# Optimization experiments

Hardware: AMD Instinct MI355X
Metric: run time of the kernel (lower is better)

Reference implementation:

```python
import jax, jax.numpy as jnp
import numpy as np

KERNEL_MUL = 2.0
KERNEL_NUM = 5


def setup_inputs() -> dict:
    key = jax.random.key(0)
    k1, k2 = jax.random.split(key)
    B, Ns, Nt, K = 4, 2048, 2048, 32
    source = jax.random.normal(k1, (B, Ns, K), dtype=jnp.float32)
    target = jax.random.normal(k2, (B, Nt, K), dtype=jnp.float32)
    return {"source": source, "target": target}


def _mmd_rbf(source, target):
    # source: [B, Ns, K], target: [B, Nt, K]
    Ns = source.shape[1]
    Nt = target.shape[1]
    n_samples = Ns + Nt
    total = jnp.concatenate([source, target], axis=1)  # [B, N, K]
    # Pairwise squared L2 via Gram trick (avoids [B, N, N, K] broadcast tensor)
    sq = jnp.sum(total * total, axis=-1)  # [B, N]
    gram = jnp.einsum('bik,bjk->bij', total, total)  # [B, N, N]
    L2 = sq[:, :, None] + sq[:, None, :] - 2.0 * gram  # [B, N, N]
    # Multi-bandwidth RBF kernel sum
    bw = jnp.sum(L2, axis=(1, 2), keepdims=True) / (n_samples ** 2 - n_samples + 1e-8)  # [B,1,1]
    bw = bw / (KERNEL_MUL ** (KERNEL_NUM // 2))
    # Small fixed loop over bandwidths; accumulate to avoid [K_num, B, N, N] stack.
    kernel = jnp.zeros_like(L2)
    for i in range(KERNEL_NUM):
        kernel = kernel + jnp.exp(-L2 / (bw * (KERNEL_MUL ** i)) + 1e-8)
    # Quadrant means
    N = Ns
    XX = kernel[:, :N, :N].mean(axis=(1, 2))
    YY = kernel[:, N:, N:].mean(axis=(1, 2))
    XY = kernel[:, :N, N:].mean(axis=(1, 2))
    YX = kernel[:, N:, :N].mean(axis=(1, 2))
    return XX + YY - XY - YX  # [B]


def reference(source, target):
    return _mmd_rbf(source, target)
```

## Files before the change

kernel.cpp:

```cpp
#include <hip/hip_runtime.h>
#include <hip/hip_bf16.h>


#define NPTS 4096
#define HALF 2048
#define KDIM 32
#define T3   128
#define NTB3 32
#define GRIDX 187
#define SPREAD 64

#define WS_SQ    0
#define WS_PART  65536
#define WS_QUAD  133120
#define WS_FRAG  147456
#define WS_NEED  (147456 + 4 * NPTS * 128)

typedef __attribute__((ext_vector_type(8))) short short8v;
typedef __attribute__((ext_vector_type(4))) float f32x4;

__device__ __forceinline__ float fast_exp2(float x) {
#if __has_builtin(__builtin_amdgcn_exp2f)
  return __builtin_amdgcn_exp2f(x);
#else
  return exp2f(x);
#endif
}

__device__ __forceinline__ unsigned int bf16_rne(float x) {
  unsigned int u = __float_as_uint(x);
  return (u + 0x7fffu + ((u >> 16) & 1u)) >> 16;
}

__device__ __forceinline__ const float* point_ptr(const float* __restrict__ src,
                                                  const float* __restrict__ tgt,
                                                  int b, int p) {
  return (p < HALF) ? src + ((size_t)b * HALF + p) * KDIM
                    : tgt + ((size_t)b * HALF + (p - HALF)) * KDIM;
}

__global__ void __launch_bounds__(64)
mmd_pass1(const float* __restrict__ src, const float* __restrict__ tgt,
          float* __restrict__ sqArr, double* __restrict__ part1,
          double* __restrict__ quadbuf,
          unsigned char* __restrict__ frags, int preFlag) {
  const int b = blockIdx.y;
  const int tid = threadIdx.x;
  const int p = blockIdx.x * 64 + tid;

  if (blockIdx.x == 0) {
#pragma unroll
    for (int i = 0; i < 4; ++i)
      quadbuf[b * 4 * SPREAD + i * 64 + tid] = 0.0;
  }

  const float* __restrict__ xp = point_ptr(src, tgt, b, p);
  float x[KDIM];
#pragma unroll
  for (int q = 0; q < 8; ++q) {
    float4 v = reinterpret_cast<const float4*>(xp)[q];
    x[4*q+0] = v.x; x[4*q+1] = v.y; x[4*q+2] = v.z; x[4*q+3] = v.w;
  }
  float s0 = 0.f, s1 = 0.f, s2 = 0.f, s3 = 0.f;
#pragma unroll
  for (int q = 0; q < 8; ++q) {
    s0 = fmaf(x[4*q+0], x[4*q+0], s0);
    s1 = fmaf(x[4*q+1], x[4*q+1], s1);
    s2 = fmaf(x[4*q+2], x[4*q+2], s2);
    s3 = fmaf(x[4*q+3], x[4*q+3], s3);
  }
  const float sq = (s0 + s1) + (s2 + s3);
  sqArr[(size_t)b * NPTS + p] = sq;

  if (preFlag) {
    unsigned int hw[16], lw[16];
#pragma unroll
    for (int e = 0; e < 16; ++e) {
      const float xa = x[2*e], xb = x[2*e+1];
      const unsigned int ha = bf16_rne(xa);
      const unsigned int la = bf16_rne(xa - __uint_as_float(ha << 16));
      const unsigned int hb = bf16_rne(xb);
      const unsigned int lb = bf16_rne(xb - __uint_as_float(hb << 16));
      hw[e] = ha | (hb << 16);
      lw[e] = la | (lb << 16);
    }
    uint4* dst = reinterpret_cast<uint4*>(frags + (size_t)(b * NPTS + p) * 128);
#pragma unroll
    for (int c = 0; c < 4; ++c)
      dst[c] = make_uint4(hw[4*c], hw[4*c+1], hw[4*c+2], hw[4*c+3]);
#pragma unroll
    for (int c = 0; c < 4; ++c)
      dst[4 + c] = make_uint4(lw[4*c], lw[4*c+1], lw[4*c+2], lw[4*c+3]);
  }

  __shared__ float lx[64][KDIM + 1];
#pragma unroll
  for (int k = 0; k < KDIM; ++k) lx[tid][k] = x[k];
  __syncthreads();

  double* slot = part1 + ((size_t)b * 64 + blockIdx.x) * 33;
  if (tid < 32) {
    float ps = 0.f;
#pragma unroll 16
    for (int r = 0; r < 64; ++r) ps += lx[r][tid];
    slot[1 + tid] = (double)ps;
  }
  float w = sq;
#pragma unroll
  for (int off = 32; off > 0; off >>= 1) w += __shfl_down(w, off, 64);
  if (tid == 0) slot[0] = (double)w;
}

__device__ __forceinline__ short8v lds_frag(const unsigned char* base, int p,
                                            int half, int lk) {
  const int slot = (half * 4 + lk) ^ (p & 7);
  return *reinterpret_cast<const short8v*>(base + p * 128 + slot * 16);
}

template <bool PRE>
__global__ void __launch_bounds__(512, 6)
mmd_pass3(const float* __restrict__ src, const float* __restrict__ tgt,
          const float* __restrict__ sqArr, const double* __restrict__ part1,
          const unsigned char* __restrict__ frags,
          double* __restrict__ quadbuf) {
  const int bid = blockIdx.x;
  const int b = blockIdx.y;
  const int tid = threadIdx.x;
  const int lane = tid & 63;
  const int w = tid >> 6;
  const int lm = lane & 15;
  const int lk = lane >> 4;
  const int wr = w & 3;
  const int wc = w >> 2;

  int rem = bid, bx = 0;
  for (;;) {
    const int nseg = (32 - bx + 2) / 3;
    if (rem < nseg) break;
    rem -= nseg; ++bx;
  }
  const int by0 = bx + rem * 3;
  const int cnt = min(3, 32 - by0);

  __shared__ __align__(16) unsigned char fragA[T3 * 128];
  __shared__ __align__(16) unsigned char fragB[2][T3 * 128];
  __shared__ float s_sqA[T3], s_sqB[2][T3];
  __shared__ double red[33];
  __shared__ float s_nc4;

  const float* __restrict__ sqG = sqArr + (size_t)b * NPTS;
  const uint4* __restrict__ gfr =
      reinterpret_cast<const uint4*>(frags) + (size_t)b * NPTS * 8;

  if (tid < 33) {
    double s = 0.0;
#pragma unroll 16
    for (int blk = 0; blk < 64; ++blk)
      s += part1[((size_t)b * 64 + blk) * 33 + tid];
    red[tid] = s;
  }
  __syncthreads();
  if (tid == 0) {
    double ssq = red[0], s2 = 0.0;
    for (int k = 1; k <= 32; ++k) s2 += red[k] * red[k];
    const double N = (double)NPTS;
    double bw = (2.0 * N * ssq - 2.0 * s2) / (N * N - N + 1e-8);
    bw *= 0.25;
    s_nc4 = (float)(-1.4426950408889634 / (bw * 16.0));
  }

  if constexpr (PRE) {
#pragma unroll
    for (int i = 0; i < 2; ++i) {
      const int g = tid + i * 512;
      const int p = g >> 3, s = g & 7;
      const int d = p * 8 + (s ^ (p & 7));
      reinterpret_cast<uint4*>(fragA)[d] = gfr[(size_t)bx * 1024 + g];
      reinterpret_cast<uint4*>(fragB[0])[d] = gfr[(size_t)by0 * 1024 + g];
    }
  } else if (tid < 256) {
    const int pt = tid & 127;
    const bool isB = tid >= 128;
    const float* fp = point_ptr(src, tgt, b, (isB ? by0 : bx) * T3 + pt);
    unsigned int hw[16], lw[16];
#pragma unroll
    for (int e = 0; e < 16; ++e) {
      const float xa = fp[2*e], xb = fp[2*e+1];
      const unsigned int ha = bf16_rne(xa);
      const unsigned int la = bf16_rne(xa - __uint_as_float(ha << 16));
      const unsigned int hb = bf16_rne(xb);
      const unsigned int lb = bf16_rne(xb - __uint_as_float(hb << 16));
      hw[e] = ha | (hb << 16);
      lw[e] = la | (lb << 16);
    }
    uint4* dst = reinterpret_cast<uint4*>((isB ? fragB[0] : fragA) + pt * 128);
#pragma unroll
    for (int s = 0; s < 8; ++s) {
      const unsigned int* s4 = (s < 4) ? &hw[s * 4] : &lw[(s - 4) * 4];
      dst[s ^ (pt & 7)] = make_uint4(s4[0], s4[1], s4[2], s4[3]);
    }
  }
  if (tid < 128) s_sqA[tid] = sqG[bx * T3 + tid];
  else if (tid < 256) s_sqB[0][tid - 128] = sqG[by0 * T3 + (tid - 128)];
  __syncthreads();

  const float nc4 = s_nc4;
  const float m2nc = -2.0f * nc4;

  short8v Ah[2], Al[2];
  float sin_[2][4];
#pragma unroll
  for (int rg = 0; rg < 2; ++rg) {
    const int pa = wr * 32 + rg * 16 + lm;
    Ah[rg] = lds_frag(fragA, pa, 0, lk);
    Al[rg] = lds_frag(fragA, pa, 1, lk);
    const float4 q4 = *reinterpret_cast<const float4*>(
        &s_sqA[wr * 32 + rg * 16 + lk * 4]);
    sin_[rg][0] = q4.x * nc4; sin_[rg][1] = q4.y * nc4;
    sin_[rg][2] = q4.z * nc4; sin_[rg][3] = q4.w * nc4;
  }

  const int rh = (bx >= NTB3 / 2) ? 1 : 0;

  for (int it = 0; it < cnt; ++it) {
    const int c = it & 1;
    const int by = by0 + it;

    uint4 pv0, pv1;
    float nsq = 0.f;
    const bool hn = (it + 1 < cnt);
    if (hn) {
      if constexpr (PRE) {
        pv0 = gfr[(size_t)(by + 1) * 1024 + tid];
        pv1 = gfr[(size_t)(by + 1) * 1024 + tid + 512];
      }
      if (tid < 128) nsq = sqG[(by + 1) * T3 + tid];
    }

    double accd = 0.0;
#pragma unroll
    for (int cg = 0; cg < 4; ++cg) {
      const int pb = wc * 64 + cg * 16 + lm;
      const short8v Bh = lds_frag(fragB[c], pb, 0, lk);
      const short8v Bl = lds_frag(fragB[c], pb, 1, lk);
      const float sjn = s_sqB[c][pb] * nc4;
#pragma unroll
      for (int rg = 0; rg < 2; ++rg) {
        f32x4 accP = {0.f, 0.f, 0.f, 0.f};
        f32x4 accQ = {0.f, 0.f, 0.f, 0.f};
        accP = __builtin_amdgcn_mfma_f32_16x16x32_bf16(Ah[rg], Bh, accP, 0, 0, 0);
        accQ = __builtin_amdgcn_mfma_f32_16x16x32_bf16(Ah[rg], Bl, accQ, 0, 0, 0);
        accP = __builtin_amdgcn_mfma_f32_16x16x32_bf16(Al[rg], Bl, accP, 0, 0, 0);
        accQ = __builtin_amdgcn_mfma_f32_16x16x32_bf16(Al[rg], Bh, accQ, 0, 0, 0);
        float rs = 0.f;
#pragma unroll
        for (int reg = 0; reg < 4; ++reg) {
          const float dot = accP[reg] + accQ[reg];
          const float arg = fmaf(dot, m2nc, sin_[rg][reg] + sjn);
          float e = fast_exp2(arg);
          float s = e;
          e *= e; s += e;
          e *= e; s += e;
          e *= e; s += e;
          e *= e; s += e;
          rs += s;
        }
        accd += (double)rs;
      }
    }

#pragma unroll
    for (int off = 32; off > 0; off >>= 1) accd += __shfl_down(accd, off, 64);
    if (lane == 0) {
      const int ch = (by >= NTB3 / 2) ? 1 : 0;
      const int q  = (rh << 1) | ch;
      const int qT = (ch << 1) | rh;
      const int slot = (bid * 8 + w) & (SPREAD - 1);
      atomicAdd(&quadbuf[(((b << 2) | q) * SPREAD) + slot], accd);
      if (bx != by)
        atomicAdd(&quadbuf[(((b << 2) | qT) * SPREAD) + slot], accd);
    }

    if (hn) {
      if constexpr (PRE) {
        {
          const int p = tid >> 3, s = tid & 7;
          reinterpret_cast<uint4*>(fragB[c ^ 1])[p * 8 + (s ^ (p & 7))] = pv0;
        }
        {
          const int g = tid + 512;
          const int p = g >> 3, s = g & 7;
          reinterpret_cast<uint4*>(fragB[c ^ 1])[p * 8 + (s ^ (p & 7))] = pv1;
        }
      } else if (tid < 128) {
        const int pt = tid;
        const float* fp = point_ptr(src, tgt, b, (by + 1) * T3 + pt);
        unsigned int hw[16], lw[16];
#pragma unroll
        for (int e = 0; e < 16; ++e) {
          const float xa = fp[2*e], xb = fp[2*e+1];
          const unsigned int ha = bf16_rne(xa);
          const unsigned int la = bf16_rne(xa - __uint_as_float(ha << 16));
          const unsigned int hb = bf16_rne(xb);
          const unsigned int lb = bf16_rne(xb - __uint_as_float(hb << 16));
          hw[e] = ha | (hb << 16);
          lw[e] = la | (lb << 16);
        }
        uint4* dst = reinterpret_cast<uint4*>(fragB[c ^ 1] + pt * 128);
#pragma unroll
        for (int s = 0; s < 8; ++s) {
          const unsigned int* s4 = (s < 4) ? &hw[s * 4] : &lw[(s - 4) * 4];
          dst[s ^ (pt & 7)] = make_uint4(s4[0], s4[1], s4[2], s4[3]);
        }
      }
      if (tid < 128) s_sqB[c ^ 1][tid] = nsq;
      __syncthreads();
    }
  }
}

__global__ void mmd_pass4(const double* __restrict__ quadbuf, float* __restrict__ out) {
  const int tid = threadIdx.x;
  const int qq = tid >> 6, i = tid & 63;
  __shared__ double wsum[4];
  const double inv = 1.0 / ((double)HALF * (double)HALF);
  for (int b = 0; b < 4; ++b) {
    double v = quadbuf[((b << 2) | qq) * SPREAD + i];
    double sv = (qq == 0 || qq == 3) ? v : -v;
#pragma unroll
    for (int off = 32; off > 0; off >>= 1) sv += __shfl_down(sv, off, 64);
    if ((tid & 63) == 0) wsum[qq] = sv;
    __syncthreads();
    if (tid == 0) out[b] = (float)((wsum[0] + wsum[1] + wsum[2] + wsum[3]) * inv);
    __syncthreads();
  }
}

extern "C" void kernel_launch(void* const* d_in, const int* in_sizes, int n_in,
                              void* d_out, int out_size, void* d_ws, size_t ws_size,
                              hipStream_t stream) {
  const float* src = (const float*)d_in[0];
  const float* tgt = (const float*)d_in[1];
  float* out = (float*)d_out;

  char* ws = (char*)d_ws;
  float*         sqArr   = (float*)(ws + WS_SQ);
  double*        part1   = (double*)(ws + WS_PART);
  double*        quadbuf = (double*)(ws + WS_QUAD);
  unsigned char* frags   = (unsigned char*)(ws + WS_FRAG);

  const int pre = (ws_size >= (size_t)WS_NEED) ? 1 : 0;

  mmd_pass1<<<dim3(64, 4), 64, 0, stream>>>(src, tgt, sqArr, part1,
                                            quadbuf, frags, pre);
  if (pre)
    mmd_pass3<true><<<dim3(GRIDX, 4), 512, 0, stream>>>(src, tgt, sqArr, part1,
                                                        frags, quadbuf);
  else
    mmd_pass3<false><<<dim3(GRIDX, 4), 512, 0, stream>>>(src, tgt, sqArr, part1,
                                                         frags, quadbuf);
  mmd_pass4<<<1, 256, 0, stream>>>(quadbuf, out);
}
```

Before: 83.97 us.

## Fold bandwidth reduction and final combine into last-block epilogues, pack exp math

Bandwidth coefficient computation moves out of every pass3 block into a last-block-done epilogue of pass1 using an atomic counter. The separate final reduction kernel is removed; the last pass3 block per batch computes the output. The exp ladder is rewritten over 2-wide float vectors to encourage packed FP32 ops. This removes a kernel launch and redundant per-block reductions, but adds a memset, atomics and threadfences.

```diff
diff --git a/kernel.cpp b/kernel.cpp
--- a/kernel.cpp
+++ b/kernel.cpp
@@ -13,11 +13,14 @@
 #define WS_SQ    0
 #define WS_PART  65536
 #define WS_QUAD  133120
+#define WS_CNT   141312
+#define WS_COEF  141344
 #define WS_FRAG  147456
 #define WS_NEED  (147456 + 4 * NPTS * 128)
 
 typedef __attribute__((ext_vector_type(8))) short short8v;
 typedef __attribute__((ext_vector_type(4))) float f32x4;
+typedef __attribute__((ext_vector_type(2))) float f32x2;
 
 __device__ __forceinline__ float fast_exp2(float x) {
 #if __has_builtin(__builtin_amdgcn_exp2f)
@@ -42,8 +45,9 @@
 __global__ void __launch_bounds__(64)
 mmd_pass1(const float* __restrict__ src, const float* __restrict__ tgt,
           float* __restrict__ sqArr, double* __restrict__ part1,
-          double* __restrict__ quadbuf,
-          unsigned char* __restrict__ frags, int preFlag) {
+          double* __restrict__ quadbuf, unsigned int* __restrict__ cnt1,
+          float* __restrict__ coef, unsigned char* __restrict__ frags,
+          int preFlag) {
   const int b = blockIdx.y;
   const int tid = threadIdx.x;
   const int p = blockIdx.x * 64 + tid;
@@ -103,12 +107,38 @@
     float ps = 0.f;
 #pragma unroll 16
     for (int r = 0; r < 64; ++r) ps += lx[r][tid];
-    slot[1 + tid] = (double)ps;
+    atomicExch(reinterpret_cast<unsigned long long*>(&slot[1 + tid]),
+               (unsigned long long)__double_as_longlong((double)ps));
   }
   float w = sq;
 #pragma unroll
   for (int off = 32; off > 0; off >>= 1) w += __shfl_down(w, off, 64);
-  if (tid == 0) slot[0] = (double)w;
+  if (tid == 0)
+    atomicExch(reinterpret_cast<unsigned long long*>(&slot[0]),
+               (unsigned long long)__double_as_longlong((double)w));
+
+  __threadfence();
+  __shared__ int s_last;
+  if (tid == 0) s_last = (atomicAdd(&cnt1[b], 1u) == 63u) ? 1 : 0;
+  __syncthreads();
+  if (s_last) {
+    __shared__ double red[33];
+    if (tid < 33) {
+      double s = 0.0;
+      for (int blk = 0; blk < 64; ++blk)
+        s += atomicAdd(&part1[((size_t)b * 64 + blk) * 33 + tid], 0.0);
+      red[tid] = s;
+    }
+    __syncthreads();
+    if (tid == 0) {
+      double ssq = red[0], s2 = 0.0;
+      for (int k = 1; k <= 32; ++k) s2 += red[k] * red[k];
+      const double N = (double)NPTS;
+      double bw = (2.0 * N * ssq - 2.0 * s2) / (N * N - N + 1e-8);
+      bw *= 0.25;
+      coef[b] = (float)(-1.4426950408889634 / (bw * 16.0));
+    }
+  }
 }
 
 __device__ __forceinline__ short8v lds_frag(const unsigned char* base, int p,
@@ -117,12 +147,25 @@
   return *reinterpret_cast<const short8v*>(base + p * 128 + slot * 16);
 }
 
+__device__ __forceinline__ f32x2 ladder2(f32x2 arg) {
+  f32x2 e;
+  e[0] = fast_exp2(arg[0]);
+  e[1] = fast_exp2(arg[1]);
+  f32x2 s = e;
+  e = e * e; s = s + e;
+  e = e * e; s = s + e;
+  e = e * e; s = s + e;
+  e = e * e; s = s + e;
+  return s;
+}
+
 template <bool PRE>
 __global__ void __launch_bounds__(512, 6)
 mmd_pass3(const float* __restrict__ src, const float* __restrict__ tgt,
-          const float* __restrict__ sqArr, const double* __restrict__ part1,
+          const float* __restrict__ sqArr, const float* __restrict__ coef,
           const unsigned char* __restrict__ frags,
-          double* __restrict__ quadbuf) {
+          double* __restrict__ quadbuf, unsigned int* __restrict__ cnt3,
+          float* __restrict__ out) {
   const int bid = blockIdx.x;
   const int b = blockIdx.y;
   const int tid = threadIdx.x;
@@ -145,29 +188,12 @@
   __shared__ __align__(16) unsigned char fragA[T3 * 128];
   __shared__ __align__(16) unsigned char fragB[2][T3 * 128];
   __shared__ float s_sqA[T3], s_sqB[2][T3];
-  __shared__ double red[33];
-  __shared__ float s_nc4;
-
+
+  const float nc4 = coef[b];
+  const float m2nc = -2.0f * nc4;
   const float* __restrict__ sqG = sqArr + (size_t)b * NPTS;
   const uint4* __restrict__ gfr =
       reinterpret_cast<const uint4*>(frags) + (size_t)b * NPTS * 8;
-
-  if (tid < 33) {
-    double s = 0.0;
-#pragma unroll 16
-    for (int blk = 0; blk < 64; ++blk)
-      s += part1[((size_t)b * 64 + blk) * 33 + tid];
-    red[tid] = s;
-  }
-  __syncthreads();
-  if (tid == 0) {
-    double ssq = red[0], s2 = 0.0;
-    for (int k = 1; k <= 32; ++k) s2 += red[k] * red[k];
-    const double N = (double)NPTS;
-    double bw = (2.0 * N * ssq - 2.0 * s2) / (N * N - N + 1e-8);
-    bw *= 0.25;
-    s_nc4 = (float)(-1.4426950408889634 / (bw * 16.0));
-  }
 
   if constexpr (PRE) {
 #pragma unroll
@@ -204,11 +230,8 @@
   else if (tid < 256) s_sqB[0][tid - 128] = sqG[by0 * T3 + (tid - 128)];
   __syncthreads();
 
-  const float nc4 = s_nc4;
-  const float m2nc = -2.0f * nc4;
-
   short8v Ah[2], Al[2];
-  float sin_[2][4];
+  f32x2 sin2[2][2];
 #pragma unroll
   for (int rg = 0; rg < 2; ++rg) {
     const int pa = wr * 32 + rg * 16 + lm;
@@ -216,11 +239,12 @@
     Al[rg] = lds_frag(fragA, pa, 1, lk);
     const float4 q4 = *reinterpret_cast<const float4*>(
         &s_sqA[wr * 32 + rg * 16 + lk * 4]);
-    sin_[rg][0] = q4.x * nc4; sin_[rg][1] = q4.y * nc4;
-    sin_[rg][2] = q4.z * nc4; sin_[rg][3] = q4.w * nc4;
+    sin2[rg][0] = f32x2{q4.x * nc4, q4.y * nc4};
+    sin2[rg][1] = f32x2{q4.z * nc4, q4.w * nc4};
   }
 
   const int rh = (bx >= NTB3 / 2) ? 1 : 0;
+  const f32x2 m2v = {m2nc, m2nc};
 
   for (int it = 0; it < cnt; ++it) {
     const int c = it & 1;
@@ -244,6 +268,7 @@
       const short8v Bh = lds_frag(fragB[c], pb, 0, lk);
       const short8v Bl = lds_frag(fragB[c], pb, 1, lk);
       const float sjn = s_sqB[c][pb] * nc4;
+      const f32x2 sjv = {sjn, sjn};
 #pragma unroll
       for (int rg = 0; rg < 2; ++rg) {
         f32x4 accP = {0.f, 0.f, 0.f, 0.f};
@@ -252,20 +277,14 @@
         accQ = __builtin_amdgcn_mfma_f32_16x16x32_bf16(Ah[rg], Bl, accQ, 0, 0, 0);
         accP = __builtin_amdgcn_mfma_f32_16x16x32_bf16(Al[rg], Bl, accP, 0, 0, 0);
         accQ = __builtin_amdgcn_mfma_f32_16x16x32_bf16(Al[rg], Bh, accQ, 0, 0, 0);
-        float rs = 0.f;
-#pragma unroll
-        for (int reg = 0; reg < 4; ++reg) {
-          const float dot = accP[reg] + accQ[reg];
-          const float arg = fmaf(dot, m2nc, sin_[rg][reg] + sjn);
-          float e = fast_exp2(arg);
-          float s = e;
-          e *= e; s += e;
-          e *= e; s += e;
-          e *= e; s += e;
-          e *= e; s += e;
-          rs += s;
-        }
-        accd += (double)rs;
+        const f32x2 pl = __builtin_shufflevector(accP, accP, 0, 1);
+        const f32x2 ph = __builtin_shufflevector(accP, accP, 2, 3);
+        const f32x2 ql = __builtin_shufflevector(accQ, accQ, 0, 1);
+        const f32x2 qh = __builtin_shufflevector(accQ, accQ, 2, 3);
+        const f32x2 al = (pl + ql) * m2v + (sin2[rg][0] + sjv);
+        const f32x2 ah = (ph + qh) * m2v + (sin2[rg][1] + sjv);
+        const f32x2 rsv = ladder2(al) + ladder2(ah);
+        accd += (double)rsv[0] + (double)rsv[1];
       }
     }
 
@@ -317,22 +336,26 @@
       __syncthreads();
     }
   }
-}
-
-__global__ void mmd_pass4(const double* __restrict__ quadbuf, float* __restrict__ out) {
-  const int tid = threadIdx.x;
-  const int qq = tid >> 6, i = tid & 63;
-  __shared__ double wsum[4];
-  const double inv = 1.0 / ((double)HALF * (double)HALF);
-  for (int b = 0; b < 4; ++b) {
-    double v = quadbuf[((b << 2) | qq) * SPREAD + i];
-    double sv = (qq == 0 || qq == 3) ? v : -v;
-#pragma unroll
-    for (int off = 32; off > 0; off >>= 1) sv += __shfl_down(sv, off, 64);
-    if ((tid & 63) == 0) wsum[qq] = sv;
+
+  __threadfence();
+  __shared__ unsigned int s_old;
+  if (tid == 0) s_old = atomicAdd(&cnt3[b], 1u);
+  __syncthreads();
+  if (s_old == GRIDX - 1) {
+    __shared__ double wq[4];
+    if (tid < 256) {
+      const int qq = tid >> 6, i = tid & 63;
+      double v = atomicAdd(&quadbuf[((b << 2) | qq) * SPREAD + i], 0.0);
+      double sv = (qq == 0 || qq == 3) ? v : -v;
+#pragma unroll
+      for (int off = 32; off > 0; off >>= 1) sv += __shfl_down(sv, off, 64);
+      if ((tid & 63) == 0) wq[qq] = sv;
+    }
     __syncthreads();
-    if (tid == 0) out[b] = (float)((wsum[0] + wsum[1] + wsum[2] + wsum[3]) * inv);
-    __syncthreads();
+    if (tid == 0) {
+      const double inv = 1.0 / ((double)HALF * (double)HALF);
+      out[b] = (float)((wq[0] + wq[1] + wq[2] + wq[3]) * inv);
+    }
   }
 }
 
@@ -347,17 +370,20 @@
   float*         sqArr   = (float*)(ws + WS_SQ);
   double*        part1   = (double*)(ws + WS_PART);
   double*        quadbuf = (double*)(ws + WS_QUAD);
+  unsigned int*  cnt1    = (unsigned int*)(ws + WS_CNT);
+  unsigned int*  cnt3    = (unsigned int*)(ws + WS_CNT + 16);
+  float*         coef    = (float*)(ws + WS_COEF);
   unsigned char* frags   = (unsigned char*)(ws + WS_FRAG);
 
   const int pre = (ws_size >= (size_t)WS_NEED) ? 1 : 0;
 
-  mmd_pass1<<<dim3(64, 4), 64, 0, stream>>>(src, tgt, sqArr, part1,
-                                            quadbuf, frags, pre);
+  hipMemsetAsync(ws + WS_CNT, 0, 32, stream);
+  mmd_pass1<<<dim3(64, 4), 64, 0, stream>>>(src, tgt, sqArr, part1, quadbuf,
+                                            cnt1, coef, frags, pre);
   if (pre)
-    mmd_pass3<true><<<dim3(GRIDX, 4), 512, 0, stream>>>(src, tgt, sqArr, part1,
-                                                        frags, quadbuf);
+    mmd_pass3<true><<<dim3(GRIDX, 4), 512, 0, stream>>>(
+        src, tgt, sqArr, coef, frags, quadbuf, cnt3, out);
   else
-    mmd_pass3<false><<<dim3(GRIDX, 4), 512, 0, stream>>>(src, tgt, sqArr, part1,
-                                                         frags, quadbuf);
-  mmd_pass4<<<1, 256, 0, stream>>>(quadbuf, out);
-}
+    mmd_pass3<false><<<dim3(GRIDX, 4), 512, 0, stream>>>(
+        src, tgt, sqArr, coef, frags, quadbuf, cnt3, out);
+}
```

Measured after the change: 169.5 us. 2.02x slower.
